# Performance work log

Hardware: AMD Instinct MI355X
Metric: run time of the kernel (lower is better)

Reference implementation:

```python
import jax, jax.numpy as jnp
import numpy as np

LN_EPS = 1e-5

def _lstm_cell(x, h, c, Wih, Whh, bih, bhh):
    # gates: [b, 4*d], PyTorch LSTMCell gate order: i, f, g, o
    gates = x @ Wih.T + bih + h @ Whh.T + bhh
    i, f, g, o = jnp.split(gates, 4, axis=-1)
    c_new = jax.nn.sigmoid(f) * c + jax.nn.sigmoid(i) * jnp.tanh(g)
    h_new = jax.nn.sigmoid(o) * jnp.tanh(c_new)
    return h_new, c_new

def _layernorm(x, g, b):
    mu = jnp.mean(x, axis=-1, keepdims=True)
    var = jnp.mean(jnp.square(x - mu), axis=-1, keepdims=True)
    return (x - mu) * jax.lax.rsqrt(var + LN_EPS) * g + b

def setup_inputs() -> dict:
    key = jax.random.key(0)
    ks = jax.random.split(key, 8)
    B, F_, L, D, V, NL = 128, 1, 32, 512, 10000, 2
    features = jax.random.normal(ks[0], (B, F_, D), dtype=jnp.float32)
    caption = jax.random.randint(ks[1], (B, L), 0, V, dtype=jnp.int64)
    emb_W = jax.random.normal(ks[2], (V, D), dtype=jnp.float32) * 0.02
    W_ih = jax.random.normal(ks[3], (NL, 4 * D, D), dtype=jnp.float32) * (1.0 / np.sqrt(D))
    W_hh = jax.random.normal(ks[4], (NL, 4 * D, D), dtype=jnp.float32) * (1.0 / np.sqrt(D))
    b_ih = jnp.zeros((NL, 4 * D), dtype=jnp.float32)
    b_hh = jnp.zeros((NL, 4 * D), dtype=jnp.float32)
    ln_g = jnp.ones((D,), dtype=jnp.float32)
    ln_b = jnp.zeros((D,), dtype=jnp.float32)
    fc_W = jax.random.normal(ks[5], (V, D), dtype=jnp.float32) * np.sqrt(2.0 / D)
    fc_b = jnp.zeros((V,), dtype=jnp.float32)
    return {"features": features, "caption": caption, "emb_W": emb_W,
            "W_ih": W_ih, "W_hh": W_hh, "b_ih": b_ih, "b_hh": b_hh,
            "ln_g": ln_g, "ln_b": ln_b, "fc_W": fc_W, "fc_b": fc_b}

def reference(features, caption, emb_W, W_ih, W_hh, b_ih, b_hh, ln_g, ln_b, fc_W, fc_b):
    b, f, d = features.shape
    n_layers = W_ih.shape[0]
    emb = emb_W[caption]                                   # [b, L, d]
    inp = jnp.concatenate([features, emb], axis=1)         # [b, T, d], T = f + L
    h0 = jnp.zeros((b, d), dtype=features.dtype)
    c0 = jnp.zeros((b, d), dtype=features.dtype)

    def step(carry, x_t):
        h, c = carry
        # Faithful to the original: every layer consumes x_t, sharing (h, c).
        for l in range(n_layers):
            h, c = _lstm_cell(x_t, h, c, W_ih[l], W_hh[l], b_ih[l], b_hh[l])
        h = _layernorm(h, ln_g, ln_b)                      # normalized h carries forward
        logits_t = h @ fc_W.T + fc_b                       # [b, V]
        return (h, c), logits_t

    xs = jnp.swapaxes(inp, 0, 1)                           # [T, b, d]
    _, logits = jax.lax.scan(step, (h0, c0), xs)           # [T, b, V]
    logits = jnp.swapaxes(logits, 0, 1)                    # [b, T, V]
    return jax.nn.log_softmax(logits[:, f:, :], axis=-1)   # [b, L, V]
```

## Files before the change

kernel.cpp:

```cpp
#include <hip/hip_runtime.h>

#define B_ 128
#define D_ 512
#define T_ 33
#define L_ 32
#define V_ 10000
#define NWG 128
#define THREADS 512

typedef short short8 __attribute__((ext_vector_type(8)));
typedef float f32x4 __attribute__((ext_vector_type(4)));

__device__ __forceinline__ short f2bf_rne(float f) {
    unsigned u = __builtin_bit_cast(unsigned, f);
    unsigned r = (u + 0x7FFFu + ((u >> 16) & 1u)) >> 16;
    return (short)r;
}
__device__ __forceinline__ void split2(float v, short& hi, short& lo) {
    unsigned u = __builtin_bit_cast(unsigned, v);
    hi = (short)(u >> 16);
    float hif = __builtin_bit_cast(float, u & 0xFFFF0000u);
    lo = (short)(__builtin_bit_cast(unsigned, v - hif) >> 16);
}
__device__ __forceinline__ float sigm(float x) {
    return 1.0f / (1.0f + __expf(-x));
}
__device__ __forceinline__ float unpack2f(unsigned u) {
    return __builtin_bit_cast(float, u << 16)
         + __builtin_bit_cast(float, u & 0xFFFF0000u);
}

__device__ __forceinline__ void llc_stu(void* p, unsigned v) {
    __hip_atomic_store((unsigned*)p, v, __ATOMIC_RELAXED,
                       __HIP_MEMORY_SCOPE_SYSTEM);
}

__global__ void prep_kernel(const float* __restrict__ features,
                            const int* __restrict__ caption,
                            const float* __restrict__ embW,
                            const float* __restrict__ fcW,
                            short* __restrict__ Xhi,
                            short* __restrict__ Xlo,
                            short* __restrict__ fcWb,
                            int* __restrict__ syncv) {
    const long NX = (long)T_ * B_ * D_;
    const long NW = (long)V_ * D_;
    const long total = NX + NW;
    long gid = (long)blockIdx.x * blockDim.x + threadIdx.x;
    if (gid < NWG) syncv[gid] = 0;
    for (long idx = gid; idx < total; idx += (long)gridDim.x * blockDim.x) {
        if (idx < NX) {
            int t = (int)(idx / (B_ * D_));
            int r = (int)(idx % (B_ * D_));
            int b = r >> 9;
            int d = r & 511;
            float v;
            if (t == 0) v = features[r];
            else        v = embW[(long)caption[b * L_ + (t - 1)] * D_ + d];
            short hi, lo;
            split2(v, hi, lo);
            Xhi[idx] = hi;
            Xlo[idx] = lo;
        } else {
            long j = idx - NX;
            fcWb[j] = f2bf_rne(fcW[j]);
        }
    }
}

__global__ __launch_bounds__(THREADS)
void lstm_persist(const short* __restrict__ Xhi, const short* __restrict__ Xlo,
                  const float* __restrict__ Wih, const float* __restrict__ Whh,
                  const float* __restrict__ bih, const float* __restrict__ bhh,
                  const float* __restrict__ lng, const float* __restrict__ lnb,
                  unsigned* __restrict__ H0p, unsigned* __restrict__ H1p,
                  short* __restrict__ Hnb, int* __restrict__ syncv) {
    __shared__ __align__(16) short Wh[2][16][1032];
    __shared__ __align__(16) short Wo[2][16][1032];
    __shared__ float gbuf[128][17];
    __shared__ float carr[128][4];
    __shared__ float rs_s[128], murs_s[128];
    __shared__ float gam_s[512], bet_s[512];
    __shared__ float bias_s[2][16];
    __shared__ float bconst_s[16];
    __shared__ float sgam_s[16];

    const int tid  = threadIdx.x;
    const int w    = blockIdx.x;
    const int d0   = w * 4;
    const int wave = tid >> 6;
    const int lane = tid & 63;
    const int wm   = wave * 16;
    const int n    = lane & 15;
    const int kq   = (lane >> 4) * 8;

    gam_s[tid & 511] = lng[tid & 511];
    bet_s[tid & 511] = lnb[tid & 511];
    if (tid < 32) {
        int l = tid >> 4, nn = tid & 15;
        int row = (nn >> 2) * 512 + d0 + (nn & 3);
        bias_s[l][nn] = bih[l * 2048 + row] + bhh[l * 2048 + row];
    }
    for (int idx = tid; idx < 2 * 16 * 1024; idx += THREADS) {
        int l = idx >> 14;
        int nn = (idx >> 10) & 15;
        int k = idx & 1023;
        int row = (nn >> 2) * 512 + d0 + (nn & 3);
        float v = (k < 512) ? Wih[((long)(l * 2048 + row)) * 512 + k]
                            : Whh[((long)(l * 2048 + row)) * 512 + (k - 512)];
        if (l == 0 && k >= 512) v *= lng[k - 512];
        short hi, lo;
        split2(v, hi, lo);
        Wh[l][nn][k] = hi;
        Wo[l][nn][k] = lo;
    }
    if (tid < 256) {
        const int c = tid >> 4, kc = tid & 15;
        const int row = (c >> 2) * 512 + d0 + (c & 3);
        float sb = 0.f, sg = 0.f;
        for (int k = kc * 32; k < kc * 32 + 32; ++k) {
            const float wv = Whh[(long)row * 512 + k];
            sb += lnb[k] * wv;
            sg += lng[k] * wv;
        }
        gbuf[c][kc]      = sb;
        gbuf[64 + c][kc] = sg;
    }
    carr[tid >> 2][tid & 3] = 0.f;
    __syncthreads();
    if (tid < 32) {
        const int c = tid & 15;
        const int base = (tid >= 16) ? 64 + c : c;
        float s = 0.f;
        for (int i = 0; i < 16; ++i) s += gbuf[base][i];
        if (tid < 16) bconst_s[c] = s;
        else          sgam_s[c]   = s;
    }
    __syncthreads();

    int* flags = syncv;
    int nb = 0;

    auto arrive = [&]() {
        __syncthreads();
        ++nb;
        if (tid == 0)
            __hip_atomic_store(&flags[w], nb, __ATOMIC_RELAXED,
                               __HIP_MEMORY_SCOPE_SYSTEM);
    };
    auto wait_bar = [&]() {
        if (wave == 0) {
            const int tgt = nb;
            int iter = 0;
            for (;;) {
                int f0 = __hip_atomic_load(&flags[lane], __ATOMIC_RELAXED,
                                           __HIP_MEMORY_SCOPE_SYSTEM);
                int f1 = __hip_atomic_load(&flags[64 + lane], __ATOMIC_RELAXED,
                                           __HIP_MEMORY_SCOPE_SYSTEM);
                if (__all(f0 >= tgt && f1 >= tgt)) break;
                if (++iter > 65536) break;
                __builtin_amdgcn_s_sleep(1);
            }
            __builtin_amdgcn_fence(__ATOMIC_ACQUIRE, "agent");
        }
        __syncthreads();
    };

    auto ln_stats = [&]() {
        const int row = tid & 127, q = tid >> 7;
        const uint4* hp = (const uint4*)&H1p[row * 512 + q * 128];
        float s = 0.f, s2 = 0.f;
        #pragma unroll 8
        for (int i = 0; i < 32; ++i) {
            uint4 u = hp[i];
            #pragma unroll
            for (int e = 0; e < 4; ++e) {
                const float v = unpack2f((&u.x)[e]);
                s  += v;
                s2 += v * v;
            }
        }
        gbuf[row][q * 2]     = s;
        gbuf[row][q * 2 + 1] = s2;
        __syncthreads();
        if (tid < 128) {
            const float ss  = gbuf[tid][0] + gbuf[tid][2] + gbuf[tid][4] + gbuf[tid][6];
            const float ss2 = gbuf[tid][1] + gbuf[tid][3] + gbuf[tid][5] + gbuf[tid][7];
            const float mu  = ss * (1.0f / 512.0f);
            const float var = ss2 * (1.0f / 512.0f) - mu * mu;
            const float rs  = rsqrtf(var + 1e-5f);
            rs_s[tid]   = rs;
            murs_s[tid] = mu * rs;
        }
        __syncthreads();
    };

    const int rA0 = (wm + n) * 512;
    const int rq  = (lane >> 4) * 4;

    for (int t = 0; t < T_; ++t) {
        const short* xh = Xhi + (long)t * B_ * D_;
        const short* xl = Xlo + (long)t * B_ * D_;

        {
            f32x4 accx = {0.f, 0.f, 0.f, 0.f};
            f32x4 acch = {0.f, 0.f, 0.f, 0.f};
            #pragma unroll 4
            for (int kc = 0; kc < 16; ++kc) {
                const int kg = kc * 32 + kq;
                short8 bh = *(const short8*)&Wh[0][n][kg];
                short8 bl = *(const short8*)&Wo[0][n][kg];
                short8 ah = *(const short8*)&xh[rA0 + kg];
                short8 al = *(const short8*)&xl[rA0 + kg];
                accx = __builtin_amdgcn_mfma_f32_16x16x32_bf16(ah, bh, accx, 0, 0, 0);
                accx = __builtin_amdgcn_mfma_f32_16x16x32_bf16(ah, bl, accx, 0, 0, 0);
                accx = __builtin_amdgcn_mfma_f32_16x16x32_bf16(al, bh, accx, 0, 0, 0);
            }
            if (t > 0) {
                wait_bar();
                #pragma unroll 4
                for (int kc = 0; kc < 16; ++kc) {
                    const int kh = kc * 32 + kq;
                    short8 bh = *(const short8*)&Wh[0][n][512 + kh];
                    short8 bl = *(const short8*)&Wo[0][n][512 + kh];
                    unsigned u[8];
                    *(uint4*)&u[0] = *(const uint4*)&H1p[rA0 + kh];
                    *(uint4*)&u[4] = *(const uint4*)&H1p[rA0 + kh + 4];
                    short8 ah, al;
                    #pragma unroll
                    for (int j = 0; j < 8; ++j) {
                        ah[j] = (short)(u[j] & 0xFFFFu);
                        al[j] = (short)(u[j] >> 16);
                    }
                    acch = __builtin_amdgcn_mfma_f32_16x16x32_bf16(ah, bh, acch, 0, 0, 0);
                    acch = __builtin_amdgcn_mfma_f32_16x16x32_bf16(ah, bl, acch, 0, 0, 0);
                    acch = __builtin_amdgcn_mfma_f32_16x16x32_bf16(al, bh, acch, 0, 0, 0);
                }
                ln_stats();
                if (w < 32 && t >= 2) {
                    const int rb = w * 4;
                    for (int idx = tid; idx < 2048; idx += THREADS) {
                        const int m = rb + (idx >> 9), k = idx & 511;
                        const float v = unpack2f(H1p[m * 512 + k]);
                        const float o = fmaf(fmaf(v, rs_s[m], -murs_s[m]), gam_s[k], bet_s[k]);
                        Hnb[(((long)(t - 2)) * B_ + m) * D_ + k] = f2bf_rne(o);
                    }
                }
            }
            const float bs = bias_s[0][n] + (t > 0 ? bconst_s[n] : 0.f);
            const float sg = sgam_s[n];
            #pragma unroll
            for (int r = 0; r < 4; ++r) {
                const int row = wm + rq + r;
                float g = accx[r] + bs;
                if (t > 0) g += acch[r] * rs_s[row] - murs_s[row] * sg;
                gbuf[row][n] = g;
            }
            __syncthreads();
            {
                const int m = tid >> 2, d = tid & 3;
                const float gi = gbuf[m][d],     gf = gbuf[m][4 + d];
                const float gg = gbuf[m][8 + d], go = gbuf[m][12 + d];
                const float cn = sigm(gf) * carr[m][d] + sigm(gi) * tanhf(gg);
                carr[m][d] = cn;
                const float hv = sigm(go) * tanhf(cn);
                short hi_, lo_;
                split2(hv, hi_, lo_);
                const unsigned pk = (unsigned)(unsigned short)hi_
                                  | ((unsigned)(unsigned short)lo_ << 16);
                llc_stu(&H0p[m * 512 + d0 + d], pk);
            }
            arrive();
        }

        {
            f32x4 acc = {0.f, 0.f, 0.f, 0.f};
            #pragma unroll 4
            for (int kc = 0; kc < 16; ++kc) {
                const int kg = kc * 32 + kq;
                short8 bh = *(const short8*)&Wh[1][n][kg];
                short8 bl = *(const short8*)&Wo[1][n][kg];
                short8 ah = *(const short8*)&xh[rA0 + kg];
                short8 al = *(const short8*)&xl[rA0 + kg];
                acc = __builtin_amdgcn_mfma_f32_16x16x32_bf16(ah, bh, acc, 0, 0, 0);
                acc = __builtin_amdgcn_mfma_f32_16x16x32_bf16(ah, bl, acc, 0, 0, 0);
                acc = __builtin_amdgcn_mfma_f32_16x16x32_bf16(al, bh, acc, 0, 0, 0);
            }
            wait_bar();
            #pragma unroll 4
            for (int kc = 0; kc < 16; ++kc) {
                const int kh = kc * 32 + kq;
                short8 bh = *(const short8*)&Wh[1][n][512 + kh];
                short8 bl = *(const short8*)&Wo[1][n][512 + kh];
                unsigned u[8];
                *(uint4*)&u[0] = *(const uint4*)&H0p[rA0 + kh];
                *(uint4*)&u[4] = *(const uint4*)&H0p[rA0 + kh + 4];
                short8 ah, al;
                #pragma unroll
                for (int j = 0; j < 8; ++j) {
                    ah[j] = (short)(u[j] & 0xFFFFu);
                    al[j] = (short)(u[j] >> 16);
                }
                acc = __builtin_amdgcn_mfma_f32_16x16x32_bf16(ah, bh, acc, 0, 0, 0);
                acc = __builtin_amdgcn_mfma_f32_16x16x32_bf16(ah, bl, acc, 0, 0, 0);
                acc = __builtin_amdgcn_mfma_f32_16x16x32_bf16(al, bh, acc, 0, 0, 0);
            }
            const float bs = bias_s[1][n];
            #pragma unroll
            for (int r = 0; r < 4; ++r)
                gbuf[wm + rq + r][n] = acc[r] + bs;
            __syncthreads();
            {
                const int m = tid >> 2, d = tid & 3;
                const float gi = gbuf[m][d],     gf = gbuf[m][4 + d];
                const float gg = gbuf[m][8 + d], go = gbuf[m][12 + d];
                const float cn = sigm(gf) * carr[m][d] + sigm(gi) * tanhf(gg);
                carr[m][d] = cn;
                const float hv = sigm(go) * tanhf(cn);
                short hi_, lo_;
                split2(hv, hi_, lo_);
                const unsigned pk = (unsigned)(unsigned short)hi_
                                  | ((unsigned)(unsigned short)lo_ << 16);
                llc_stu(&H1p[m * 512 + d0 + d], pk);
            }
            arrive();
        }
    }

    wait_bar();
    ln_stats();
    if (w < 32) {
        const int rb = w * 4;
        for (int idx = tid; idx < 2048; idx += THREADS) {
            const int m = rb + (idx >> 9), k = idx & 511;
            const float v = unpack2f(H1p[m * 512 + k]);
            const float o = fmaf(fmaf(v, rs_s[m], -murs_s[m]), gam_s[k], bet_s[k]);
            Hnb[(((long)(L_ - 1)) * B_ + m) * D_ + k] = f2bf_rne(o);
        }
    }
}

__launch_bounds__(256)
__global__ void gemm_fc(const short* __restrict__ A,
                        const short* __restrict__ Wt,
                        const float* __restrict__ bias,
                        float* __restrict__ out) {
    __shared__ __align__(16) short As[128 * 40];
    __shared__ __align__(16) short Bs[128 * 40];
    const int tid = threadIdx.x;
    const int m0 = blockIdx.x * 128;
    const int n0 = blockIdx.y * 128;
    const int lrow = tid >> 1;
    const int lcol = (tid & 1) * 16;
    const int w = tid >> 6;
    const int lane = tid & 63;
    const int wm = (w >> 1) * 64;
    const int wn = (w & 1) * 64;

    f32x4 acc[4][4];
    #pragma unroll
    for (int i = 0; i < 4; ++i)
        #pragma unroll
        for (int j = 0; j < 4; ++j)
            acc[i][j] = (f32x4){0.f, 0.f, 0.f, 0.f};

    for (int kc = 0; kc < 16; ++kc) {
        const int kg = kc * 32;
        {
            const float4* src = reinterpret_cast<const float4*>(
                A + (long)(m0 + lrow) * D_ + kg + lcol);
            float4 v0 = src[0];
            float4 v1 = src[1];
            float4* dst = reinterpret_cast<float4*>(&As[lrow * 40 + lcol]);
            dst[0] = v0;
            dst[1] = v1;
        }
        {
            const int nn = n0 + lrow;
            float4 v0 = {0.f, 0.f, 0.f, 0.f}, v1 = {0.f, 0.f, 0.f, 0.f};
            if (nn < V_) {
                const float4* src = reinterpret_cast<const float4*>(
                    Wt + (long)nn * D_ + kg + lcol);
                v0 = src[0];
                v1 = src[1];
            }
            float4* dst = reinterpret_cast<float4*>(&Bs[lrow * 40 + lcol]);
            dst[0] = v0;
            dst[1] = v1;
        }
        __syncthreads();
        const int kcol = (lane >> 4) * 8;
        const int rsel = lane & 15;
        short8 a[4], bf[4];
        #pragma unroll
        for (int i = 0; i < 4; ++i)
            a[i] = *reinterpret_cast<const short8*>(&As[(wm + i * 16 + rsel) * 40 + kcol]);
        #pragma unroll
        for (int j = 0; j < 4; ++j)
            bf[j] = *reinterpret_cast<const short8*>(&Bs[(wn + j * 16 + rsel) * 40 + kcol]);
        #pragma unroll
        for (int i = 0; i < 4; ++i)
            #pragma unroll
            for (int j = 0; j < 4; ++j)
                acc[i][j] = __builtin_amdgcn_mfma_f32_16x16x32_bf16(a[i], bf[j], acc[i][j], 0, 0, 0);
        __syncthreads();
    }

    const int rquad = (lane >> 4) * 4;
    const int ncol = lane & 15;
    #pragma unroll
    for (int i = 0; i < 4; ++i) {
        #pragma unroll
        for (int j = 0; j < 4; ++j) {
            const int ngl = n0 + wn + j * 16 + ncol;
            if (ngl < V_) {
                const float bv = bias[ngl];
                #pragma unroll
                for (int r = 0; r < 4; ++r) {
                    const int mgl = m0 + wm + i * 16 + rquad + r;
                    const int tt = mgl >> 7;
                    const int bb = mgl & 127;
                    out[((long)bb * L_ + tt) * V_ + ngl] = acc[i][j][r] + bv;
                }
            }
        }
    }
}

__global__ void logsoftmax_kernel(float* __restrict__ out) {
    __shared__ float red[256];
    const long row = blockIdx.x;
    float* p = out + row * V_;
    float4* p4 = reinterpret_cast<float4*>(p);
    const int tid = threadIdx.x;
    float s = 0.f;
    for (int i = tid; i < V_ / 4; i += 256) {
        float4 v = p4[i];
        s += __expf(v.x) + __expf(v.y) + __expf(v.z) + __expf(v.w);
    }
    red[tid] = s;
    __syncthreads();
    for (int st = 128; st > 0; st >>= 1) {
        if (tid < st) red[tid] += red[tid + st];
        __syncthreads();
    }
    const float ls = logf(red[0]);
    for (int i = tid; i < V_ / 4; i += 256) {
        float4 v = p4[i];
        v.x -= ls; v.y -= ls; v.z -= ls; v.w -= ls;
        p4[i] = v;
    }
}

extern "C" void kernel_launch(void* const* d_in, const int* in_sizes, int n_in,
                              void* d_out, int out_size, void* d_ws, size_t ws_size,
                              hipStream_t stream) {
    const float* features = (const float*)d_in[0];
    const int*   caption  = (const int*)d_in[1];
    const float* embW     = (const float*)d_in[2];
    const float* W_ih     = (const float*)d_in[3];
    const float* W_hh     = (const float*)d_in[4];
    const float* b_ih     = (const float*)d_in[5];
    const float* b_hh     = (const float*)d_in[6];
    const float* ln_g     = (const float*)d_in[7];
    const float* ln_b     = (const float*)d_in[8];
    const float* fc_W     = (const float*)d_in[9];
    const float* fc_b     = (const float*)d_in[10];
    float* out = (float*)d_out;

    char* ws = (char*)d_ws;
    int*      syncv = (int*)ws;      ws += 512;
    short*    Xhi   = (short*)ws;    ws += (size_t)T_ * B_ * D_ * 2;
    short*    Xlo   = (short*)ws;    ws += (size_t)T_ * B_ * D_ * 2;
    unsigned* H0p   = (unsigned*)ws; ws += (size_t)B_ * D_ * 4;
    unsigned* H1p   = (unsigned*)ws; ws += (size_t)B_ * D_ * 4;
    short*    Hnb   = (short*)ws;    ws += (size_t)L_ * B_ * D_ * 2;
    short*    fcWb  = (short*)ws;    ws += (size_t)V_ * D_ * 2;

    prep_kernel<<<2048, 256, 0, stream>>>(features, caption, embW, fc_W,
                                          Xhi, Xlo, fcWb, syncv);

    lstm_persist<<<NWG, THREADS, 0, stream>>>(Xhi, Xlo, W_ih, W_hh, b_ih, b_hh,
                                              ln_g, ln_b, H0p, H1p, Hnb,
                                              syncv);

    gemm_fc<<<dim3(32, 79), 256, 0, stream>>>(Hnb, fcWb, fc_b, out);
    logsoftmax_kernel<<<4096, 256, 0, stream>>>(out);
}
```

Before: 1.674 ms.

## Fuse FC GEMM into persistent LSTM kernel via flag-gated helper workgroups

```diff
diff --git a/kernel.cpp b/kernel.cpp
--- a/kernel.cpp
+++ b/kernel.cpp
@@ -6,10 +6,15 @@
 #define L_ 32
 #define V_ 10000
 #define NWG 128
+#define NHELP 128
 #define THREADS 512
+#define NTILE_M 32
+#define NTILE_N 79
 
 typedef short short8 __attribute__((ext_vector_type(8)));
 typedef float f32x4 __attribute__((ext_vector_type(4)));
+typedef unsigned uint32x4 __attribute__((ext_vector_type(4)));
+typedef unsigned uint32x2 __attribute__((ext_vector_type(2)));
 
 __device__ __forceinline__ short f2bf_rne(float f) {
     unsigned u = __builtin_bit_cast(unsigned, f);
@@ -33,6 +38,22 @@
 __device__ __forceinline__ void llc_stu(void* p, unsigned v) {
     __hip_atomic_store((unsigned*)p, v, __ATOMIC_RELAXED,
                        __HIP_MEMORY_SCOPE_SYSTEM);
+}
+__device__ __forceinline__ uint32x4 llc_ld4(const void* p) {
+    uint32x4 r;
+    asm volatile("global_load_dwordx4 %0, %1, off sc0 sc1"
+                 : "=v"(r) : "v"(p));
+    return r;
+}
+__device__ __forceinline__ uint32x2 llc_ld2(const void* p) {
+    uint32x2 r;
+    asm volatile("global_load_dwordx2 %0, %1, off sc0 sc1"
+                 : "=v"(r) : "v"(p));
+    return r;
+}
+__device__ __forceinline__ void llc_wait() {
+    asm volatile("s_waitcnt vmcnt(0)" ::: "memory");
+    __builtin_amdgcn_sched_barrier(0);
 }
 
 __global__ void prep_kernel(const float* __restrict__ features,
@@ -74,7 +95,9 @@
                   const float* __restrict__ bih, const float* __restrict__ bhh,
                   const float* __restrict__ lng, const float* __restrict__ lnb,
                   unsigned* __restrict__ H0p, unsigned* __restrict__ H1p,
-                  short* __restrict__ Hnb, int* __restrict__ syncv) {
+                  short* __restrict__ Hnb, int* __restrict__ syncv,
+                  const short* __restrict__ fcWb, const float* __restrict__ fcb,
+                  float* __restrict__ out) {
     __shared__ __align__(16) short Wh[2][16][1032];
     __shared__ __align__(16) short Wo[2][16][1032];
     __shared__ float gbuf[128][17];
@@ -86,13 +109,119 @@
     __shared__ float sgam_s[16];
 
     const int tid  = threadIdx.x;
-    const int w    = blockIdx.x;
-    const int d0   = w * 4;
     const int wave = tid >> 6;
     const int lane = tid & 63;
-    const int wm   = wave * 16;
-    const int n    = lane & 15;
-    const int kq   = (lane >> 4) * 8;
+    int* flags = syncv;
+
+    if (blockIdx.x >= NWG) {
+        const int h = blockIdx.x - NWG;
+        short* As = (short*)&Wh[0][0][0];
+        short* Bs = As + 2 * 128 * 40;
+        const int lrow  = tid >> 2;
+        const int lcol  = (tid & 3) * 8;
+        const int wavem = (wave >> 2) * 64;
+        const int waven = (wave & 3) * 32;
+        const int rsel  = lane & 15;
+        const int kcol  = (lane >> 4) * 8;
+        const int rquad = (lane >> 4) * 4;
+        const int ncol  = lane & 15;
+
+        for (int tau = h; tau < NTILE_M * NTILE_N; tau += NHELP) {
+            const int mt = tau / NTILE_N;
+            const int nt = tau - mt * NTILE_N;
+            const int m0 = mt * 128, n0 = nt * 128;
+            if (wave == 0) {
+                const int tgt = 2 * mt + 5;
+                int it2 = 0;
+                for (;;) {
+                    int f0 = __hip_atomic_load(&flags[lane], __ATOMIC_RELAXED,
+                                               __HIP_MEMORY_SCOPE_SYSTEM);
+                    int f1 = __hip_atomic_load(&flags[64 + lane], __ATOMIC_RELAXED,
+                                               __HIP_MEMORY_SCOPE_SYSTEM);
+                    if (__all(f0 >= tgt && f1 >= tgt)) break;
+                    if (++it2 > (1 << 20)) break;
+                    __builtin_amdgcn_s_sleep(8);
+                }
+            }
+            __syncthreads();
+
+            f32x4 acc[4][2];
+            #pragma unroll
+            for (int i = 0; i < 4; ++i)
+                #pragma unroll
+                for (int j = 0; j < 2; ++j)
+                    acc[i][j] = (f32x4){0.f, 0.f, 0.f, 0.f};
+
+            const short* Ab = Hnb + (long)(m0 + lrow) * D_ + lcol;
+            const int nrow = n0 + lrow;
+            const short* Bb = fcWb + (long)nrow * D_ + lcol;
+            const bool bok = nrow < V_;
+
+            uint32x4 va = llc_ld4(Ab);
+            uint32x4 vb = 0;
+            if (bok) vb = llc_ld4(Bb);
+            llc_wait();
+            *(uint32x4*)&As[lrow * 40 + lcol] = va;
+            *(uint32x4*)&Bs[lrow * 40 + lcol] = vb;
+            uint32x4 va2 = llc_ld4(Ab + 32);
+            uint32x4 vb2 = 0;
+            if (bok) vb2 = llc_ld4(Bb + 32);
+            __syncthreads();
+
+            for (int kc = 0; kc < 16; ++kc) {
+                const int bo = (kc & 1) * 5120;
+                short8 a[4], bw[2];
+                #pragma unroll
+                for (int i = 0; i < 4; ++i)
+                    a[i] = *(const short8*)&As[bo + (wavem + i * 16 + rsel) * 40 + kcol];
+                #pragma unroll
+                for (int j = 0; j < 2; ++j)
+                    bw[j] = *(const short8*)&Bs[bo + (waven + j * 16 + rsel) * 40 + kcol];
+                #pragma unroll
+                for (int i = 0; i < 4; ++i)
+                    #pragma unroll
+                    for (int j = 0; j < 2; ++j)
+                        acc[i][j] = __builtin_amdgcn_mfma_f32_16x16x32_bf16(a[i], bw[j], acc[i][j], 0, 0, 0);
+                if (kc + 1 < 16) {
+                    llc_wait();
+                    const int b1 = ((kc + 1) & 1) * 5120;
+                    *(uint32x4*)&As[b1 + lrow * 40 + lcol] = va2;
+                    *(uint32x4*)&Bs[b1 + lrow * 40 + lcol] = vb2;
+                    if (kc + 2 < 16) {
+                        va2 = llc_ld4(Ab + (kc + 2) * 32);
+                        vb2 = 0;
+                        if (bok) vb2 = llc_ld4(Bb + (kc + 2) * 32);
+                    }
+                }
+                __syncthreads();
+            }
+
+            #pragma unroll
+            for (int i = 0; i < 4; ++i) {
+                #pragma unroll
+                for (int j = 0; j < 2; ++j) {
+                    const int ngl = n0 + waven + j * 16 + ncol;
+                    if (ngl < V_) {
+                        const float bv = fcb[ngl];
+                        #pragma unroll
+                        for (int r = 0; r < 4; ++r) {
+                            const int mgl = m0 + wavem + i * 16 + rquad + r;
+                            const int tt = mgl >> 7;
+                            const int bb = mgl & 127;
+                            out[((long)bb * L_ + tt) * V_ + ngl] = acc[i][j][r] + bv;
+                        }
+                    }
+                }
+            }
+        }
+        return;
+    }
+
+    const int w  = blockIdx.x;
+    const int d0 = w * 4;
+    const int wm = wave * 16;
+    const int n  = lane & 15;
+    const int kq = (lane >> 4) * 8;
 
     gam_s[tid & 511] = lng[tid & 511];
     bet_s[tid & 511] = lnb[tid & 511];
@@ -138,7 +267,6 @@
     }
     __syncthreads();
 
-    int* flags = syncv;
     int nb = 0;
 
     auto arrive = [&]() {
@@ -161,23 +289,29 @@
                 if (++iter > 65536) break;
                 __builtin_amdgcn_s_sleep(1);
             }
-            __builtin_amdgcn_fence(__ATOMIC_ACQUIRE, "agent");
         }
         __syncthreads();
     };
 
     auto ln_stats = [&]() {
         const int row = tid & 127, q = tid >> 7;
-        const uint4* hp = (const uint4*)&H1p[row * 512 + q * 128];
+        const unsigned* hp = &H1p[row * 512 + q * 128];
         float s = 0.f, s2 = 0.f;
-        #pragma unroll 8
-        for (int i = 0; i < 32; ++i) {
-            uint4 u = hp[i];
-            #pragma unroll
-            for (int e = 0; e < 4; ++e) {
-                const float v = unpack2f((&u.x)[e]);
-                s  += v;
-                s2 += v * v;
+        #pragma unroll
+        for (int c = 0; c < 2; ++c) {
+            uint32x4 sb[16];
+            #pragma unroll
+            for (int i = 0; i < 16; ++i)
+                sb[i] = llc_ld4(hp + c * 64 + i * 4);
+            llc_wait();
+            #pragma unroll
+            for (int i = 0; i < 16; ++i) {
+                #pragma unroll
+                for (int e = 0; e < 4; ++e) {
+                    const float v = unpack2f(sb[i][e]);
+                    s  += v;
+                    s2 += v * v;
+                }
             }
         }
         gbuf[row][q * 2]     = s;
@@ -193,6 +327,33 @@
             murs_s[tid] = mu * rs;
         }
         __syncthreads();
+    };
+
+    unsigned* Hnb32 = (unsigned*)Hnb;
+    auto mat_slot = [&](int slot) {
+        const int rb = w * 4;
+        const int p0 = tid, p1 = tid + 512;
+        const int m0r = rb + (p0 >> 8), k0 = (p0 & 255) * 2;
+        const int m1r = rb + (p1 >> 8), k1 = (p1 & 255) * 2;
+        uint32x2 a = llc_ld2(&H1p[m0r * 512 + k0]);
+        uint32x2 b = llc_ld2(&H1p[m1r * 512 + k1]);
+        llc_wait();
+        {
+            const float v0 = unpack2f(a[0]), v1 = unpack2f(a[1]);
+            const float o0 = fmaf(fmaf(v0, rs_s[m0r], -murs_s[m0r]), gam_s[k0],     bet_s[k0]);
+            const float o1 = fmaf(fmaf(v1, rs_s[m0r], -murs_s[m0r]), gam_s[k0 + 1], bet_s[k0 + 1]);
+            const unsigned pk = (unsigned)(unsigned short)f2bf_rne(o0)
+                              | ((unsigned)(unsigned short)f2bf_rne(o1) << 16);
+            llc_stu(&Hnb32[((long)slot * B_ + m0r) * 256 + (p0 & 255)], pk);
+        }
+        {
+            const float v0 = unpack2f(b[0]), v1 = unpack2f(b[1]);
+            const float o0 = fmaf(fmaf(v0, rs_s[m1r], -murs_s[m1r]), gam_s[k1],     bet_s[k1]);
+            const float o1 = fmaf(fmaf(v1, rs_s[m1r], -murs_s[m1r]), gam_s[k1 + 1], bet_s[k1 + 1]);
+            const unsigned pk = (unsigned)(unsigned short)f2bf_rne(o0)
+                              | ((unsigned)(unsigned short)f2bf_rne(o1) << 16);
+            llc_stu(&Hnb32[((long)slot * B_ + m1r) * 256 + (p1 & 255)], pk);
+        }
     };
 
     const int rA0 = (wm + n) * 512;
@@ -218,34 +379,37 @@
             }
             if (t > 0) {
                 wait_bar();
-                #pragma unroll 4
-                for (int kc = 0; kc < 16; ++kc) {
-                    const int kh = kc * 32 + kq;
-                    short8 bh = *(const short8*)&Wh[0][n][512 + kh];
-                    short8 bl = *(const short8*)&Wo[0][n][512 + kh];
-                    unsigned u[8];
-                    *(uint4*)&u[0] = *(const uint4*)&H1p[rA0 + kh];
-                    *(uint4*)&u[4] = *(const uint4*)&H1p[rA0 + kh + 4];
-                    short8 ah, al;
+                #pragma unroll
+                for (int half = 0; half < 2; ++half) {
+                    uint32x4 hb[16];
                     #pragma unroll
-                    for (int j = 0; j < 8; ++j) {
-                        ah[j] = (short)(u[j] & 0xFFFFu);
-                        al[j] = (short)(u[j] >> 16);
+                    for (int i = 0; i < 8; ++i) {
+                        const int kh = (half * 8 + i) * 32 + kq;
+                        hb[i * 2]     = llc_ld4(&H1p[rA0 + kh]);
+                        hb[i * 2 + 1] = llc_ld4(&H1p[rA0 + kh + 4]);
                     }
-                    acch = __builtin_amdgcn_mfma_f32_16x16x32_bf16(ah, bh, acch, 0, 0, 0);
-                    acch = __builtin_amdgcn_mfma_f32_16x16x32_bf16(ah, bl, acch, 0, 0, 0);
-                    acch = __builtin_amdgcn_mfma_f32_16x16x32_bf16(al, bh, acch, 0, 0, 0);
+                    llc_wait();
+                    #pragma unroll
+                    for (int i = 0; i < 8; ++i) {
+                        const int kh = (half * 8 + i) * 32 + kq;
+                        short8 bh = *(const short8*)&Wh[0][n][512 + kh];
+                        short8 bl = *(const short8*)&Wo[0][n][512 + kh];
+                        unsigned u[8];
+                        *(uint32x4*)&u[0] = hb[i * 2];
+                        *(uint32x4*)&u[4] = hb[i * 2 + 1];
+                        short8 ah, al;
+                        #pragma unroll
+                        for (int j = 0; j < 8; ++j) {
+                            ah[j] = (short)(u[j] & 0xFFFFu);
+                            al[j] = (short)(u[j] >> 16);
+                        }
+                        acch = __builtin_amdgcn_mfma_f32_16x16x32_bf16(ah, bh, acch, 0, 0, 0);
+                        acch = __builtin_amdgcn_mfma_f32_16x16x32_bf16(ah, bl, acch, 0, 0, 0);
+                        acch = __builtin_amdgcn_mfma_f32_16x16x32_bf16(al, bh, acch, 0, 0, 0);
+                    }
                 }
                 ln_stats();
-                if (w < 32 && t >= 2) {
-                    const int rb = w * 4;
-                    for (int idx = tid; idx < 2048; idx += THREADS) {
-                        const int m = rb + (idx >> 9), k = idx & 511;
-                        const float v = unpack2f(H1p[m * 512 + k]);
-                        const float o = fmaf(fmaf(v, rs_s[m], -murs_s[m]), gam_s[k], bet_s[k]);
-                        Hnb[(((long)(t - 2)) * B_ + m) * D_ + k] = f2bf_rne(o);
-                    }
-                }
+                if (w < 32 && t >= 2) mat_slot(t - 2);
             }
             const float bs = bias_s[0][n] + (t > 0 ? bconst_s[n] : 0.f);
             const float sg = sgam_s[n];
@@ -287,23 +451,34 @@
                 acc = __builtin_amdgcn_mfma_f32_16x16x32_bf16(al, bh, acc, 0, 0, 0);
             }
             wait_bar();
-            #pragma unroll 4
-            for (int kc = 0; kc < 16; ++kc) {
-                const int kh = kc * 32 + kq;
-                short8 bh = *(const short8*)&Wh[1][n][512 + kh];
-                short8 bl = *(const short8*)&Wo[1][n][512 + kh];
-                unsigned u[8];
-                *(uint4*)&u[0] = *(const uint4*)&H0p[rA0 + kh];
-                *(uint4*)&u[4] = *(const uint4*)&H0p[rA0 + kh + 4];
-                short8 ah, al;
-                #pragma unroll
-                for (int j = 0; j < 8; ++j) {
-                    ah[j] = (short)(u[j] & 0xFFFFu);
-                    al[j] = (short)(u[j] >> 16);
-                }
-                acc = __builtin_amdgcn_mfma_f32_16x16x32_bf16(ah, bh, acc, 0, 0, 0);
-                acc = __builtin_amdgcn_mfma_f32_16x16x32_bf16(ah, bl, acc, 0, 0, 0);
-                acc = __builtin_amdgcn_mfma_f32_16x16x32_bf16(al, bh, acc, 0, 0, 0);
+            #pragma unroll
+            for (int half = 0; half < 2; ++half) {
+                uint32x4 hb[16];
+                #pragma unroll
+                for (int i = 0; i < 8; ++i) {
+                    const int kh = (half * 8 + i) * 32 + kq;
+                    hb[i * 2]     = llc_ld4(&H0p[rA0 + kh]);
+                    hb[i * 2 + 1] = llc_ld4(&H0p[rA0 + kh + 4]);
+                }
+                llc_wait();
+                #pragma unroll
+                for (int i = 0; i < 8; ++i) {
+                    const int kh = (half * 8 + i) * 32 + kq;
+                    short8 bh = *(const short8*)&Wh[1][n][512 + kh];
+                    short8 bl = *(const short8*)&Wo[1][n][512 + kh];
+                    unsigned u[8];
+                    *(uint32x4*)&u[0] = hb[i * 2];
+                    *(uint32x4*)&u[4] = hb[i * 2 + 1];
+                    short8 ah, al;
+                    #pragma unroll
+                    for (int j = 0; j < 8; ++j) {
+                        ah[j] = (short)(u[j] & 0xFFFFu);
+                        al[j] = (short)(u[j] >> 16);
+                    }
+                    acc = __builtin_amdgcn_mfma_f32_16x16x32_bf16(ah, bh, acc, 0, 0, 0);
+                    acc = __builtin_amdgcn_mfma_f32_16x16x32_bf16(ah, bl, acc, 0, 0, 0);
+                    acc = __builtin_amdgcn_mfma_f32_16x16x32_bf16(al, bh, acc, 0, 0, 0);
+                }
             }
             const float bs = bias_s[1][n];
             #pragma unroll
@@ -329,102 +504,8 @@
 
     wait_bar();
     ln_stats();
-    if (w < 32) {
-        const int rb = w * 4;
-        for (int idx = tid; idx < 2048; idx += THREADS) {
-            const int m = rb + (idx >> 9), k = idx & 511;
-            const float v = unpack2f(H1p[m * 512 + k]);
-            const float o = fmaf(fmaf(v, rs_s[m], -murs_s[m]), gam_s[k], bet_s[k]);
-            Hnb[(((long)(L_ - 1)) * B_ + m) * D_ + k] = f2bf_rne(o);
-        }
-    }
-}
-
-__launch_bounds__(256)
-__global__ void gemm_fc(const short* __restrict__ A,
-                        const short* __restrict__ Wt,
-                        const float* __restrict__ bias,
-                        float* __restrict__ out) {
-    __shared__ __align__(16) short As[128 * 40];
-    __shared__ __align__(16) short Bs[128 * 40];
-    const int tid = threadIdx.x;
-    const int m0 = blockIdx.x * 128;
-    const int n0 = blockIdx.y * 128;
-    const int lrow = tid >> 1;
-    const int lcol = (tid & 1) * 16;
-    const int w = tid >> 6;
-    const int lane = tid & 63;
-    const int wm = (w >> 1) * 64;
-    const int wn = (w & 1) * 64;
-
-    f32x4 acc[4][4];
-    #pragma unroll
-    for (int i = 0; i < 4; ++i)
-        #pragma unroll
-        for (int j = 0; j < 4; ++j)
-            acc[i][j] = (f32x4){0.f, 0.f, 0.f, 0.f};
-
-    for (int kc = 0; kc < 16; ++kc) {
-        const int kg = kc * 32;
-        {
-            const float4* src = reinterpret_cast<const float4*>(
-                A + (long)(m0 + lrow) * D_ + kg + lcol);
-            float4 v0 = src[0];
-            float4 v1 = src[1];
-            float4* dst = reinterpret_cast<float4*>(&As[lrow * 40 + lcol]);
-            dst[0] = v0;
-            dst[1] = v1;
-        }
-        {
-            const int nn = n0 + lrow;
-            float4 v0 = {0.f, 0.f, 0.f, 0.f}, v1 = {0.f, 0.f, 0.f, 0.f};
-            if (nn < V_) {
-                const float4* src = reinterpret_cast<const float4*>(
-                    Wt + (long)nn * D_ + kg + lcol);
-                v0 = src[0];
-                v1 = src[1];
-            }
-            float4* dst = reinterpret_cast<float4*>(&Bs[lrow * 40 + lcol]);
-            dst[0] = v0;
-            dst[1] = v1;
-        }
-        __syncthreads();
-        const int kcol = (lane >> 4) * 8;
-        const int rsel = lane & 15;
-        short8 a[4], bf[4];
-        #pragma unroll
-        for (int i = 0; i < 4; ++i)
-            a[i] = *reinterpret_cast<const short8*>(&As[(wm + i * 16 + rsel) * 40 + kcol]);
-        #pragma unroll
-        for (int j = 0; j < 4; ++j)
-            bf[j] = *reinterpret_cast<const short8*>(&Bs[(wn + j * 16 + rsel) * 40 + kcol]);
-        #pragma unroll
-        for (int i = 0; i < 4; ++i)
-            #pragma unroll
-            for (int j = 0; j < 4; ++j)
-                acc[i][j] = __builtin_amdgcn_mfma_f32_16x16x32_bf16(a[i], bf[j], acc[i][j], 0, 0, 0);
-        __syncthreads();
-    }
-
-    const int rquad = (lane >> 4) * 4;
-    const int ncol = lane & 15;
-    #pragma unroll
-    for (int i = 0; i < 4; ++i) {
-        #pragma unroll
-        for (int j = 0; j < 4; ++j) {
-            const int ngl = n0 + wn + j * 16 + ncol;
-            if (ngl < V_) {
-                const float bv = bias[ngl];
-                #pragma unroll
-                for (int r = 0; r < 4; ++r) {
-                    const int mgl = m0 + wm + i * 16 + rquad + r;
-                    const int tt = mgl >> 7;
-                    const int bb = mgl & 127;
-                    out[((long)bb * L_ + tt) * V_ + ngl] = acc[i][j][r] + bv;
-                }
-            }
-        }
-    }
+    if (w < 32) mat_slot(L_ - 1);
+    arrive();
 }
 
 __global__ void logsoftmax_kernel(float* __restrict__ out) {
@@ -480,10 +561,9 @@
     prep_kernel<<<2048, 256, 0, stream>>>(features, caption, embW, fc_W,
                                           Xhi, Xlo, fcWb, syncv);
 
-    lstm_persist<<<NWG, THREADS, 0, stream>>>(Xhi, Xlo, W_ih, W_hh, b_ih, b_hh,
-                                              ln_g, ln_b, H0p, H1p, Hnb,
-                                              syncv);
-
-    gemm_fc<<<dim3(32, 79), 256, 0, stream>>>(Hnb, fcWb, fc_b, out);
+    lstm_persist<<<NWG + NHELP, THREADS, 0, stream>>>(
+        Xhi, Xlo, W_ih, W_hh, b_ih, b_hh, ln_g, ln_b,
+        H0p, H1p, Hnb, syncv, fcWb, fc_b, out);
+
     logsoftmax_kernel<<<4096, 256, 0, stream>>>(out);
 }
```

New measurement: 1.802 ms. +7.6%, slower.
